# Optimization experiments

Measured on AMD Instinct MI355X. Metric: run time of the kernel, lower is better.

The kernel has to match this reference:

```python
import jax, jax.numpy as jnp
import numpy as np

N_NODES = 50000
N_EDGES = 800000
NUM_GRAPHS = 512


def setup_inputs() -> dict:
    key = jax.random.key(0)
    ks = jax.random.split(key, 6)
    x = jax.random.normal(ks[0], (N_NODES, 64), dtype=jnp.float32)
    edge_index = jax.random.randint(ks[1], (2, N_EDGES), 0, N_NODES, dtype=jnp.int64)
    batch = jnp.sort(jax.random.randint(ks[2], (N_NODES,), 0, NUM_GRAPHS, dtype=jnp.int64))
    # Glorot-ish init for the two GCNConv linear layers
    W1 = jax.random.normal(ks[3], (64, 128), dtype=jnp.float32) * (1.0 / np.sqrt(64))
    b1 = jnp.zeros((128,), dtype=jnp.float32)
    W2 = jax.random.normal(ks[4], (128, 64), dtype=jnp.float32) * (1.0 / np.sqrt(128))
    b2 = jnp.zeros((64,), dtype=jnp.float32)
    return {"x": x, "edge_index": edge_index, "batch": batch,
            "W1": W1, "b1": b1, "W2": W2, "b2": b2, "num_graphs": NUM_GRAPHS}


def _gcn_conv(x, src, dst, norm, W, b, n_nodes):
    """PyG GCNConv: out[i] = sum_{j->i} norm_ji * (x_j @ W) + b.
    src/dst/norm already include self-loops and symmetric normalization."""
    h = x @ W                                   # [N, F_out] small GEMM
    msg = h[src] * norm[:, None]                # gather + scale  [E+N, F_out]
    out = jax.ops.segment_sum(msg, dst, num_segments=n_nodes)  # scatter-add
    return out + b


def reference(x, edge_index, batch, W1, b1, W2, b2, num_graphs):
    n = x.shape[0]
    loops = jnp.arange(n, dtype=edge_index.dtype)
    src = jnp.concatenate([edge_index[0], loops])   # add self-loops
    dst = jnp.concatenate([edge_index[1], loops])
    # symmetric normalization D^{-1/2} (A+I) D^{-1/2}
    deg = jax.ops.segment_sum(jnp.ones_like(dst, dtype=x.dtype), dst, num_segments=n)
    dinv = jnp.where(deg > 0, jax.lax.rsqrt(deg), 0.0)
    norm = dinv[src] * dinv[dst]                    # [E+N]

    h = _gcn_conv(x, src, dst, norm, W1, b1, n)
    h = jax.nn.relu(h)
    h = _gcn_conv(h, src, dst, norm, W2, b2, n)

    # global_mean_pool over graphs
    sums = jax.ops.segment_sum(h, batch, num_segments=num_graphs)
    counts = jax.ops.segment_sum(jnp.ones((n,), dtype=h.dtype), batch, num_segments=num_graphs)
    return sums / jnp.maximum(counts, 1.0)[:, None]   # [num_graphs, out_channels]
```

## Files before the change

### kernel.cpp

```cpp
#include <hip/hip_runtime.h>

typedef unsigned short ushort_t;
typedef unsigned int uint_t;
typedef _Float16 f16;
typedef _Float16 f16x8 __attribute__((ext_vector_type(8)));
typedef float f32x4 __attribute__((ext_vector_type(4)));

constexpr int N    = 50000;
constexpr int E    = 800000;
constexpr int G    = 512;
constexpr int CAP  = 64;
constexpr int NBE  = (E + 255) / 256;
constexpr int NB8  = N / 8;

__global__ void k_zero(int4* __restrict__ p) {
    int i = blockIdx.x * blockDim.x + threadIdx.x;
    if (i < 12500) p[i] = int4{0, 0, 0, 0};
}

__global__ void k_deg(const int* __restrict__ dst, int* __restrict__ edeg,
                      ushort_t* __restrict__ rank) {
    int e = blockIdx.x * blockDim.x + threadIdx.x;
    if (e < E) rank[e] = (ushort_t)atomicAdd(&edeg[dst[e]], 1);
}

__global__ __launch_bounds__(256) void k_scatter(const int* __restrict__ src,
                                                 const int* __restrict__ dst,
                                                 const ushort_t* __restrict__ rank,
                                                 ushort_t* __restrict__ csr,
                                                 const float* __restrict__ W1,
                                                 const float* __restrict__ W2,
                                                 f16* __restrict__ W1f,
                                                 f16* __restrict__ W2f) {
    int b = blockIdx.x, t = threadIdx.x;
    if (b >= NBE) {
        int idx = (b - NBE) * 256 + t;
        if (idx < 8192) {
            int j = idx & 7, lane = (idx >> 3) & 63, c = (idx >> 9) & 7, kk = idx >> 12;
            int k = 32 * kk + 8 * (lane >> 4) + j, col = 16 * c + (lane & 15);
            W1f[idx] = (f16)W1[k * 128 + col];
        } else {
            int t2 = idx - 8192;
            int j = t2 & 7, lane = (t2 >> 3) & 63, c = (t2 >> 9) & 3, kk = (t2 >> 11) & 3;
            int k = 32 * kk + 8 * (lane >> 4) + j, col = 16 * c + (lane & 15);
            W2f[t2] = (f16)W2[k * 64 + col];
        }
        return;
    }
    int e = b * 256 + t;
    if (e >= E) return;
    int r = min((int)rank[e], CAP - 1);
    csr[(size_t)dst[e] * CAP + r] = (ushort_t)src[e];
}

__global__ __launch_bounds__(256) void k_fin(const int* __restrict__ edeg,
                                             float* __restrict__ dinv,
                                             const float* __restrict__ x,
                                             f16* __restrict__ xd) {
    int wv = threadIdx.x >> 6, lane = threadIdx.x & 63;
    int i = blockIdx.x * 4 + wv;
    if (i >= N) return;
    float di = rsqrtf(1.0f + (float)edeg[i]);
    if (lane == 0) dinv[i] = di;
    xd[(size_t)i * 64 + lane] = (f16)(di * x[(size_t)i * 64 + lane]);
}

template <bool BIAS>
__global__ __launch_bounds__(256) void k_agg(const f16* __restrict__ tbl,
                                             const int* __restrict__ edeg,
                                             const ushort_t* __restrict__ csr,
                                             const float* __restrict__ dinv,
                                             const float* __restrict__ bias,
                                             f16* __restrict__ outh) {
    int wv = threadIdx.x >> 6, l = threadIdx.x & 63;
    int g = l >> 5, sub = (l >> 3) & 3, fp = l & 7;
    int node = blockIdx.x * 8 + wv * 2 + g;
    int beg = node * CAP;
    int end = beg + min(edeg[node], CAP);
    const f16x8* tv = (const f16x8*)tbl;
    f16x8 sv = tv[(size_t)node * 8 + fp];
    float a[8] = {0.f, 0.f, 0.f, 0.f, 0.f, 0.f, 0.f, 0.f};

    int e = beg;
    for (; e + 16 <= end; e += 16) {
        int s0 = csr[e + sub];
        int s1 = csr[e + sub + 4];
        int s2 = csr[e + sub + 8];
        int s3 = csr[e + sub + 12];
        f16x8 v0 = tv[(size_t)s0 * 8 + fp];
        f16x8 v1 = tv[(size_t)s1 * 8 + fp];
        f16x8 v2 = tv[(size_t)s2 * 8 + fp];
        f16x8 v3 = tv[(size_t)s3 * 8 + fp];
#pragma unroll
        for (int j = 0; j < 8; ++j)
            a[j] += ((float)v0[j] + (float)v1[j]) + ((float)v2[j] + (float)v3[j]);
    }
    if (e < end) {
        int last = end - 1;
        int i0 = e + sub, i1 = e + sub + 4, i2 = e + sub + 8, i3 = e + sub + 12;
        int s0 = csr[min(i0, last)];
        int s1 = csr[min(i1, last)];
        int s2 = csr[min(i2, last)];
        int s3 = csr[min(i3, last)];
        f16x8 v0 = tv[(size_t)s0 * 8 + fp];
        f16x8 v1 = tv[(size_t)s1 * 8 + fp];
        f16x8 v2 = tv[(size_t)s2 * 8 + fp];
        f16x8 v3 = tv[(size_t)s3 * 8 + fp];
        float m0 = i0 < end ? 1.f : 0.f;
        float m1 = i1 < end ? 1.f : 0.f;
        float m2 = i2 < end ? 1.f : 0.f;
        float m3 = i3 < end ? 1.f : 0.f;
#pragma unroll
        for (int j = 0; j < 8; ++j)
            a[j] += (m0 * (float)v0[j] + m1 * (float)v1[j]) +
                    (m2 * (float)v2[j] + m3 * (float)v3[j]);
    }
#pragma unroll
    for (int j = 0; j < 8; ++j) {
        a[j] += __shfl_xor(a[j], 8, 64);
        a[j] += __shfl_xor(a[j], 16, 64);
    }
    float di = dinv[node];
    if (sub == 0) {
        f16x8 o;
#pragma unroll
        for (int j = 0; j < 8; ++j) {
            float r = di * ((float)sv[j] + a[j]);
            if (BIAS) r += bias[fp * 8 + j];
            o[j] = (f16)r;
        }
        *(f16x8*)(outh + (size_t)node * 64 + fp * 8) = o;
    }
}

__global__ __launch_bounds__(256) void k_gemm_mfma(const f16* __restrict__ xab,
                                                   const f16* __restrict__ W1f,
                                                   const float* __restrict__ b1,
                                                   const f16* __restrict__ W2f,
                                                   const float* __restrict__ dinv,
                                                   f16* __restrict__ h2d) {
    __shared__ f16 H1[64 * 128];
    int t = threadIdx.x;
    int w = t >> 6, l = t & 63;
    int q = l >> 4, m = l & 15;
    int n0 = blockIdx.x * 64;
    int rbase = 16 * w;

    f16x8 afr0, afr1;
    {
        int row = n0 + rbase + m;
        if (row >= N) row = N - 1;
        const f16* rp_ = xab + (size_t)row * 64 + q * 8;
        afr0 = *(const f16x8*)(rp_);
        afr1 = *(const f16x8*)(rp_ + 32);
    }
    f32x4 acc[8];
#pragma unroll
    for (int c = 0; c < 8; ++c) acc[c] = (f32x4){0.f, 0.f, 0.f, 0.f};
    const f16x8* W1v = (const f16x8*)W1f;
#pragma unroll
    for (int c = 0; c < 8; ++c) {
        f16x8 b0 = W1v[(0 * 8 + c) * 64 + l];
        f16x8 b1v = W1v[(1 * 8 + c) * 64 + l];
        acc[c] = __builtin_amdgcn_mfma_f32_16x16x32_f16(afr0, b0, acc[c], 0, 0, 0);
        acc[c] = __builtin_amdgcn_mfma_f32_16x16x32_f16(afr1, b1v, acc[c], 0, 0, 0);
    }
#pragma unroll
    for (int c = 0; c < 8; ++c) {
        float bias = b1[16 * c + m];
#pragma unroll
        for (int r = 0; r < 4; ++r) {
            int row = rbase + 4 * q + r;
            int col = 16 * c + m;
            float hv = fmaxf(acc[c][r] + bias, 0.f);
            int addr = row * 256 + col * 2;
            addr ^= ((row & 3) << 4) ^ (((row >> 2) & 3) << 5);
            *(f16*)((char*)H1 + addr) = (f16)hv;
        }
    }
    f16x8 a2[4];
#pragma unroll
    for (int kk = 0; kk < 4; ++kk) {
        int row = rbase + m;
        int addr = row * 256 + kk * 64 + q * 16;
        addr ^= ((row & 3) << 4) ^ (((row >> 2) & 3) << 5);
        a2[kk] = *(const f16x8*)((char*)H1 + addr);
    }
    f32x4 acc2[4];
#pragma unroll
    for (int c = 0; c < 4; ++c) acc2[c] = (f32x4){0.f, 0.f, 0.f, 0.f};
    const f16x8* W2v = (const f16x8*)W2f;
#pragma unroll
    for (int c = 0; c < 4; ++c) {
#pragma unroll
        for (int kk = 0; kk < 4; ++kk) {
            f16x8 b = W2v[(kk * 4 + c) * 64 + l];
            acc2[c] = __builtin_amdgcn_mfma_f32_16x16x32_f16(a2[kk], b, acc2[c], 0, 0, 0);
        }
    }
#pragma unroll
    for (int r = 0; r < 4; ++r) {
        int n = n0 + rbase + 4 * q + r;
        if (n < N) {
            float di = dinv[n];
#pragma unroll
            for (int c = 0; c < 4; ++c)
                h2d[(size_t)n * 64 + 16 * c + m] = (f16)(di * acc2[c][r]);
        }
    }
}

__global__ __launch_bounds__(256) void k_pool(const f16* __restrict__ o2h,
                                              const int* __restrict__ batch,
                                              float* __restrict__ out) {
    __shared__ float red[256];
    int g = blockIdx.x;
    int wv = threadIdx.x >> 6, lane = threadIdx.x & 63;
    int lo = 0, hi = N;
    while (lo < hi) { int m = (lo + hi) >> 1; if (batch[m] < g) lo = m + 1; else hi = m; }
    int start = lo;
    hi = N;
    while (lo < hi) { int m = (lo + hi) >> 1; if (batch[m] < g + 1) lo = m + 1; else hi = m; }
    int end = lo;
    float acc = 0.f;
    for (int n = start + wv; n < end; n += 4) acc += (float)o2h[(size_t)n * 64 + lane];
    red[threadIdx.x] = acc;
    __syncthreads();
    if (wv == 0) {
        float v = red[lane] + red[64 + lane] + red[128 + lane] + red[192 + lane];
        out[g * 64 + lane] = v / fmaxf((float)(end - start), 1.f);
    }
}

extern "C" void kernel_launch(void* const* d_in, const int* in_sizes, int n_in,
                              void* d_out, int out_size, void* d_ws, size_t ws_size,
                              hipStream_t stream) {
    const float* x     = (const float*)d_in[0];
    const int*   ei    = (const int*)d_in[1];
    const int*   batch = (const int*)d_in[2];
    const float* W1    = (const float*)d_in[3];
    const float* b1    = (const float*)d_in[4];
    const float* W2    = (const float*)d_in[5];
    const float* b2    = (const float*)d_in[6];
    float* out = (float*)d_out;

    const int* srcp = ei;
    const int* dstp = ei + E;

    char* ws = (char*)d_ws;
    int*      edeg   = (int*)     (ws + 0);
    ushort_t* rank16 = (ushort_t*)(ws + 200704);
    float*    dinv   = (float*)   (ws + 1801216);
    ushort_t* csr    = (ushort_t*)(ws + 2001920);
    f16*      xd     = (f16*)     (ws + 8401920);
    f16*      xab    = (f16*)     (ws + 14801920);
    f16*      h2d    = (f16*)     (ws + 21201920);
    f16*      o2h    = xd;
    f16*      W1f    = (f16*)     (ws + 27601920);
    f16*      W2f    = (f16*)     (ws + 27618304);

    dim3 B(256);

    k_zero<<<dim3(49), B, 0, stream>>>((int4*)edeg);
    k_deg<<<dim3(NBE), B, 0, stream>>>(dstp, edeg, rank16);
    k_scatter<<<dim3(NBE + 64), B, 0, stream>>>(srcp, dstp, rank16, csr, W1, W2, W1f, W2f);
    k_fin<<<dim3((N + 3) / 4), B, 0, stream>>>(edeg, dinv, x, xd);

    k_agg<false><<<dim3(NB8), B, 0, stream>>>(xd, edeg, csr, dinv, nullptr, xab);
    k_gemm_mfma<<<dim3((N + 63) / 64), B, 0, stream>>>(xab, W1f, b1, W2f, dinv, h2d);
    k_agg<true><<<dim3(NB8), B, 0, stream>>>(h2d, edeg, csr, dinv, b2, o2h);
    k_pool<<<dim3(G), B, 0, stream>>>(o2h, batch, out);
}
```

Measured before the change: 120.6 us.

## Merge degree-finalize into scatter kernel, vectorize degree counting, split pooling blocks

```diff
diff --git a/kernel.cpp b/kernel.cpp
--- a/kernel.cpp
+++ b/kernel.cpp
@@ -11,17 +11,25 @@
 constexpr int G    = 512;
 constexpr int CAP  = 64;
 constexpr int NBE  = (E + 255) / 256;
+constexpr int NBF  = (N + 3) / 4;
 constexpr int NB8  = N / 8;
 
-__global__ void k_zero(int4* __restrict__ p) {
+__global__ void k_zero(int4* __restrict__ edeg4, int4* __restrict__ out4) {
     int i = blockIdx.x * blockDim.x + threadIdx.x;
-    if (i < 12500) p[i] = int4{0, 0, 0, 0};
-}
-
-__global__ void k_deg(const int* __restrict__ dst, int* __restrict__ edeg,
-                      ushort_t* __restrict__ rank) {
-    int e = blockIdx.x * blockDim.x + threadIdx.x;
-    if (e < E) rank[e] = (ushort_t)atomicAdd(&edeg[dst[e]], 1);
+    if (i < 12500) edeg4[i] = int4{0, 0, 0, 0};
+    else if (i < 12500 + 8192) out4[i - 12500] = int4{0, 0, 0, 0};
+}
+
+__global__ void k_deg(const int4* __restrict__ dst4, int* __restrict__ edeg,
+                      uint2* __restrict__ rank2) {
+    int i = blockIdx.x * blockDim.x + threadIdx.x;
+    if (i >= E / 4) return;
+    int4 d = dst4[i];
+    uint_t r0 = (uint_t)atomicAdd(&edeg[d.x], 1);
+    uint_t r1 = (uint_t)atomicAdd(&edeg[d.y], 1);
+    uint_t r2 = (uint_t)atomicAdd(&edeg[d.z], 1);
+    uint_t r3 = (uint_t)atomicAdd(&edeg[d.w], 1);
+    rank2[i] = make_uint2(r0 | (r1 << 16), r2 | (r3 << 16));
 }
 
 __global__ __launch_bounds__(256) void k_scatter(const int* __restrict__ src,
@@ -31,9 +39,18 @@
                                                  const float* __restrict__ W1,
                                                  const float* __restrict__ W2,
                                                  f16* __restrict__ W1f,
-                                                 f16* __restrict__ W2f) {
+                                                 f16* __restrict__ W2f,
+                                                 const int* __restrict__ edeg,
+                                                 float* __restrict__ dinv,
+                                                 const float* __restrict__ x,
+                                                 f16* __restrict__ xd) {
     int b = blockIdx.x, t = threadIdx.x;
-    if (b >= NBE) {
+    if (b < NBE) {
+        int e = b * 256 + t;
+        if (e >= E) return;
+        int r = min((int)rank[e], CAP - 1);
+        csr[(size_t)dst[e] * CAP + r] = (ushort_t)src[e];
+    } else if (b < NBE + 64) {
         int idx = (b - NBE) * 256 + t;
         if (idx < 8192) {
             int j = idx & 7, lane = (idx >> 3) & 63, c = (idx >> 9) & 7, kk = idx >> 12;
@@ -45,24 +62,14 @@
             int k = 32 * kk + 8 * (lane >> 4) + j, col = 16 * c + (lane & 15);
             W2f[t2] = (f16)W2[k * 64 + col];
         }
-        return;
-    }
-    int e = b * 256 + t;
-    if (e >= E) return;
-    int r = min((int)rank[e], CAP - 1);
-    csr[(size_t)dst[e] * CAP + r] = (ushort_t)src[e];
-}
-
-__global__ __launch_bounds__(256) void k_fin(const int* __restrict__ edeg,
-                                             float* __restrict__ dinv,
-                                             const float* __restrict__ x,
-                                             f16* __restrict__ xd) {
-    int wv = threadIdx.x >> 6, lane = threadIdx.x & 63;
-    int i = blockIdx.x * 4 + wv;
-    if (i >= N) return;
-    float di = rsqrtf(1.0f + (float)edeg[i]);
-    if (lane == 0) dinv[i] = di;
-    xd[(size_t)i * 64 + lane] = (f16)(di * x[(size_t)i * 64 + lane]);
+    } else {
+        int wv = t >> 6, lane = t & 63;
+        int i = (b - NBE - 64) * 4 + wv;
+        if (i >= N) return;
+        float di = rsqrtf(1.0f + (float)edeg[i]);
+        if (lane == 0) dinv[i] = di;
+        xd[(size_t)i * 64 + lane] = (f16)(di * x[(size_t)i * 64 + lane]);
+    }
 }
 
 template <bool BIAS>
@@ -214,7 +221,7 @@
                                               const int* __restrict__ batch,
                                               float* __restrict__ out) {
     __shared__ float red[256];
-    int g = blockIdx.x;
+    int g = blockIdx.x >> 2, qq = blockIdx.x & 3;
     int wv = threadIdx.x >> 6, lane = threadIdx.x & 63;
     int lo = 0, hi = N;
     while (lo < hi) { int m = (lo + hi) >> 1; if (batch[m] < g) lo = m + 1; else hi = m; }
@@ -223,12 +230,14 @@
     while (lo < hi) { int m = (lo + hi) >> 1; if (batch[m] < g + 1) lo = m + 1; else hi = m; }
     int end = lo;
     float acc = 0.f;
-    for (int n = start + wv; n < end; n += 4) acc += (float)o2h[(size_t)n * 64 + lane];
+    for (int n = start + qq * 4 + wv; n < end; n += 16)
+        acc += (float)o2h[(size_t)n * 64 + lane];
     red[threadIdx.x] = acc;
     __syncthreads();
     if (wv == 0) {
         float v = red[lane] + red[64 + lane] + red[128 + lane] + red[192 + lane];
-        out[g * 64 + lane] = v / fmaxf((float)(end - start), 1.f);
+        float invc = 1.0f / fmaxf((float)(end - start), 1.f);
+        atomicAdd(&out[g * 64 + lane], v * invc);
     }
 }
 
@@ -261,13 +270,15 @@
 
     dim3 B(256);
 
-    k_zero<<<dim3(49), B, 0, stream>>>((int4*)edeg);
-    k_deg<<<dim3(NBE), B, 0, stream>>>(dstp, edeg, rank16);
-    k_scatter<<<dim3(NBE + 64), B, 0, stream>>>(srcp, dstp, rank16, csr, W1, W2, W1f, W2f);
-    k_fin<<<dim3((N + 3) / 4), B, 0, stream>>>(edeg, dinv, x, xd);
+    k_zero<<<dim3(81), B, 0, stream>>>((int4*)edeg, (int4*)out);
+    k_deg<<<dim3((E / 4 + 255) / 256), B, 0, stream>>>((const int4*)dstp, edeg,
+                                                       (uint2*)rank16);
+    k_scatter<<<dim3(NBE + 64 + NBF), B, 0, stream>>>(srcp, dstp, rank16, csr,
+                                                      W1, W2, W1f, W2f,
+                                                      edeg, dinv, x, xd);
 
     k_agg<false><<<dim3(NB8), B, 0, stream>>>(xd, edeg, csr, dinv, nullptr, xab);
     k_gemm_mfma<<<dim3((N + 63) / 64), B, 0, stream>>>(xab, W1f, b1, W2f, dinv, h2d);
     k_agg<true><<<dim3(NB8), B, 0, stream>>>(h2d, edeg, csr, dinv, b2, o2h);
-    k_pool<<<dim3(G), B, 0, stream>>>(o2h, batch, out);
-}
+    k_pool<<<dim3(G * 4), B, 0, stream>>>(o2h, batch, out);
+}
```

Measured after the change: 113.0 us. 1.07x faster.
